# Performance work log

Measured on AMD Instinct MI355X. Metric: run time of the kernel, lower is better.

Reference implementation:

```python
import jax, jax.numpy as jnp
import numpy as np

N_NODES = 50000
HEADS = 3
NEG_SLOPE = 0.2


def gat_conv(h, src, dst, W, al, ar, activation):
    # h: [N, in_dim]; W: [in_dim, H*F]; al, ar: [H, F]
    H, F = al.shape
    feat = (h @ W).reshape(N_NODES, H, F)              # [N, H, F]
    el = jnp.einsum('nhf,hf->nh', feat, al)            # [N, H]
    er = jnp.einsum('nhf,hf->nh', feat, ar)            # [N, H]
    e = jax.nn.leaky_relu(el[src] + er[dst], NEG_SLOPE)  # [E, H]
    # segment softmax over incoming edges of each dst node
    emax = jax.ops.segment_max(e, dst, num_segments=N_NODES)  # [N, H]
    ex = jnp.exp(e - emax[dst])                        # [E, H]
    denom = jax.ops.segment_sum(ex, dst, num_segments=N_NODES)  # [N, H]
    alpha = ex / denom[dst]                            # [E, H]
    msg = feat[src] * alpha[:, :, None]                # [E, H, F]
    out = jax.ops.segment_sum(msg, dst, num_segments=N_NODES)   # [N, H, F]
    if activation is not None:
        out = activation(out)
    return out


def setup_inputs() -> dict:
    key = jax.random.key(0)
    ks = jax.random.split(key, 12)
    n_edges = 1_600_000
    in_dim, hid, heads, n_cls = 256, 64, 3, 40
    d1 = hid * heads  # 192

    def glorot(k, shape):
        fan = shape[0] + shape[-1]
        return jax.random.normal(k, shape, dtype=jnp.float32) * jnp.sqrt(2.0 / fan)

    return {
        'x': jax.random.normal(ks[0], (N_NODES, in_dim), dtype=jnp.float32),
        'src': jax.random.randint(ks[1], (n_edges,), 0, N_NODES),
        'dst': jax.random.randint(ks[2], (n_edges,), 0, N_NODES),
        'W0': glorot(ks[3], (in_dim, heads * hid)),
        'al0': glorot(ks[4], (heads, hid)),
        'ar0': glorot(ks[5], (heads, hid)),
        'W1': glorot(ks[6], (d1, heads * hid)),
        'al1': glorot(ks[7], (heads, hid)),
        'ar1': glorot(ks[8], (heads, hid)),
        'W2': glorot(ks[9], (d1, heads * n_cls)),
        'al2': glorot(ks[10], (heads, n_cls)),
        'ar2': glorot(ks[11], (heads, n_cls)),
    }


def reference(x, src, dst, W0, al0, ar0, W1, al1, ar1, W2, al2, ar2):
    h = gat_conv(x, src, dst, W0, al0, ar0, jax.nn.relu)
    h = h.reshape(N_NODES, -1)  # flatten heads: [N, H*F]
    h = gat_conv(h, src, dst, W1, al1, ar1, jax.nn.relu)
    h = h.reshape(N_NODES, -1)
    logits = gat_conv(h, src, dst, W2, al2, ar2, None).mean(axis=1)  # [N, n_cls]
    return logits
```

## Files before the change

kernel.cpp:

```cpp
#include <hip/hip_runtime.h>

#define NNODES 50000
#define HEADS 3
#define NBUCK 196
#define BCAP  16320

typedef __attribute__((ext_vector_type(8))) short bf16x8;
typedef __attribute__((ext_vector_type(4))) float f32x4;

__device__ __forceinline__ float wred_sum(float v){
  #pragma unroll
  for (int s = 32; s > 0; s >>= 1) v += __shfl_xor(v, s, 64);
  return v;
}
__device__ __forceinline__ unsigned short f2bf(float x){
  unsigned int u = __float_as_uint(x);
  unsigned int r = (u + 0x7FFFu + ((u >> 16) & 1u)) >> 16;
  return (unsigned short)r;
}

__global__ __launch_bounds__(256) void prep_b_all_kernel(
    const float* __restrict__ W0, const float* __restrict__ al0, const float* __restrict__ ar0,
    const float* __restrict__ W1, const float* __restrict__ al1, const float* __restrict__ ar1,
    const float* __restrict__ W2, const float* __restrict__ al2, const float* __restrict__ ar2,
    unsigned short* __restrict__ BfAll)
{
  const int layer = blockIdx.y;
  const float *W, *al, *ar;
  int K, NT, NCf, F; unsigned short* Bf;
  if (layer == 0) { W=W0; al=al0; ar=ar0; K=256; NT=13; NCf=192; F=64; Bf=BfAll; }
  else if (layer == 1) { W=W1; al=al1; ar=ar1; K=192; NT=13; NCf=192; F=64; Bf=BfAll+53248; }
  else { W=W2; al=al2; ar=ar2; K=192; NT=8; NCf=120; F=40; Bf=BfAll+93184; }

  int tid = blockIdx.x * 256 + threadIdx.x;
  int total = (K >> 5) * NT * 64;
  if (tid >= total) return;
  int l  = tid & 63;
  int t  = (tid >> 6) % NT;
  int kc = tid / (NT * 64);
  int k0  = kc * 32 + (l >> 4) * 8;
  int col = t * 16 + (l & 15);
  unsigned short o[8];
  #pragma unroll
  for (int j = 0; j < 8; ++j) {
    int k = k0 + j;
    float v = 0.f;
    if (col < NCf) {
      v = W[(size_t)k * NCf + col];
    } else if (col < NCf + 6) {
      int c = col - NCf;
      int h = (c < 3) ? c : c - 3;
      const float* av = ((c < 3) ? al : ar) + h * F;
      const float* wp = W + (size_t)k * NCf + h * F;
      float a = 0.f;
      for (int f = 0; f < F; ++f) a += wp[f] * av[f];
      v = a;
    }
    o[j] = f2bf(v);
  }
  ushort4* dst = (ushort4*)&Bf[(size_t)tid * 8];
  dst[0] = make_ushort4(o[0], o[1], o[2], o[3]);
  dst[1] = make_ushort4(o[4], o[5], o[6], o[7]);
}

template<int AF32>
__global__ __launch_bounds__(256) void gemm_mfma_kernel(
    const void* __restrict__ Ap, const unsigned short* __restrict__ Bf,
    unsigned short* __restrict__ Cb, float* __restrict__ elp, float* __restrict__ erp,
    int M, int K, int NT, int NCf)
{
  const int w = threadIdx.x >> 6, l = threadIdx.x & 63;
  const int lrow = l & 15, kg = l >> 4;
  const int r0 = blockIdx.x * 64;
  const bf16x8* Bfv = (const bf16x8*)Bf;

  f32x4 acc[4][4];
  #pragma unroll
  for (int mt = 0; mt < 4; ++mt)
    #pragma unroll
    for (int j = 0; j < 4; ++j)
      acc[mt][j] = (f32x4){0.f, 0.f, 0.f, 0.f};

  const int nkc = K >> 5;

#define LOAD_AF(DST, KC) { \
    _Pragma("unroll") \
    for (int mt = 0; mt < 4; ++mt) { \
      int row = r0 + mt * 16 + lrow; \
      bf16x8 z = {0,0,0,0,0,0,0,0}; \
      DST[mt] = z; \
      if (row < M) { \
        if (AF32) { \
          const float* Af = (const float*)Ap; \
          const float4 v0 = *(const float4*)&Af[(size_t)row * K + (KC) * 32 + kg * 8]; \
          const float4 v1 = *(const float4*)&Af[(size_t)row * K + (KC) * 32 + kg * 8 + 4]; \
          bf16x8 a; \
          a[0] = (short)f2bf(v0.x); a[1] = (short)f2bf(v0.y); \
          a[2] = (short)f2bf(v0.z); a[3] = (short)f2bf(v0.w); \
          a[4] = (short)f2bf(v1.x); a[5] = (short)f2bf(v1.y); \
          a[6] = (short)f2bf(v1.z); a[7] = (short)f2bf(v1.w); \
          DST[mt] = a; \
        } else { \
          const unsigned short* Ab = (const unsigned short*)Ap; \
          DST[mt] = *(const bf16x8*)&Ab[(size_t)row * K + (KC) * 32 + kg * 8]; \
        } \
      } \
    } }

  bf16x8 af[4], afn[4];
  LOAD_AF(af, 0)
  for (int kc = 0; kc < nkc; ++kc) {
    if (kc + 1 < nkc) LOAD_AF(afn, kc + 1)
    #pragma unroll
    for (int j = 0; j < 4; ++j) {
      int tile = w + 4 * j;
      if (tile < NT) {
        bf16x8 bfr = Bfv[((size_t)kc * NT + tile) * 64 + l];
        #pragma unroll
        for (int mt = 0; mt < 4; ++mt)
          acc[mt][j] = __builtin_amdgcn_mfma_f32_16x16x32_bf16(af[mt], bfr, acc[mt][j], 0, 0, 0);
      }
    }
    #pragma unroll
    for (int mt = 0; mt < 4; ++mt) af[mt] = afn[mt];
  }
#undef LOAD_AF

  #pragma unroll
  for (int j = 0; j < 4; ++j) {
    int tile = w + 4 * j;
    if (tile >= NT) continue;
    int c = tile * 16 + lrow;
    #pragma unroll
    for (int mt = 0; mt < 4; ++mt) {
      #pragma unroll
      for (int rr = 0; rr < 4; ++rr) {
        int row = r0 + mt * 16 + kg * 4 + rr;
        float v = acc[mt][j][rr];
        float v1 = __shfl_xor(v, 1, 64);
        unsigned p01 = (unsigned)f2bf(v) | ((unsigned)f2bf(v1) << 16);
        unsigned p23 = __shfl_xor(p01, 2, 64);
        if (row < M) {
          if ((lrow & 3) == 0 && c + 3 < NCf)
            *(uint2*)&Cb[(size_t)row * NCf + c] = make_uint2(p01, p23);
          else if (c >= NCf && c < NCf + 3)       elp[row * 4 + (c - NCf)] = v;
          else if (c >= NCf + 3 && c < NCf + 6)   erp[row * 4 + (c - NCf - 3)] = v;
        }
      }
    }
  }
}

__global__ __launch_bounds__(256) void partition_kernel(
    const int* __restrict__ src, const int* __restrict__ dst,
    int* __restrict__ bcur, uint2* __restrict__ ebuf, int E)
{
  __shared__ int hist[NBUCK];
  __shared__ int gbase[NBUCK];
  const int t = threadIdx.x;
  const int e0 = blockIdx.x * 2048;
  for (int i = t; i < NBUCK; i += 256) hist[i] = 0;
  __syncthreads();
  int  b_[8], r_[8];
  uint2 p_[8];
  #pragma unroll
  for (int v = 0; v < 8; ++v) {
    int e = e0 + v * 256 + t;
    b_[v] = -1;
    if (e < E) {
      int s = src[e], d = dst[e];
      p_[v] = make_uint2((unsigned)s, (unsigned)d);
      b_[v] = d >> 8;
      r_[v] = atomicAdd(&hist[b_[v]], 1);
    }
  }
  __syncthreads();
  for (int i = t; i < NBUCK; i += 256) {
    int h = hist[i];
    gbase[i] = h ? atomicAdd(&bcur[i], h) : 0;
  }
  __syncthreads();
  #pragma unroll
  for (int v = 0; v < 8; ++v)
    if (b_[v] >= 0)
      ebuf[(size_t)b_[v] * BCAP + gbase[b_[v]] + r_[v]] = p_[v];
}

__global__ __launch_bounds__(256) void fill_local_kernel(
    const uint2* __restrict__ ebuf, const int* __restrict__ bcur,
    int* __restrict__ off, int* __restrict__ adj, int N)
{
  __shared__ int lhist[256], loff[256], lcur[256];
  __shared__ int wsum[4];
  __shared__ int sbase;
  const int b = blockIdx.x;
  const int t = threadIdx.x;
  const int wv = t >> 6, l = t & 63;
  const int cnt = bcur[b];
  const uint2* seg = ebuf + (size_t)b * BCAP;

  {
    int v = (t < NBUCK) ? bcur[t] : 0;
    int x = v;
    #pragma unroll
    for (int s = 1; s < 64; s <<= 1) {
      int y = __shfl_up(x, s, 64);
      if (l >= s) x += y;
    }
    if (l == 63) wsum[wv] = x;
    lhist[t] = 0; lcur[t] = 0;
    __syncthreads();
    int woff = 0;
    #pragma unroll
    for (int k = 0; k < 4; ++k) woff += (k < wv) ? wsum[k] : 0;
    if (t == b) sbase = woff + x - v;
  }
  __syncthreads();

  for (int i = t; i < cnt; i += 256)
    atomicAdd(&lhist[seg[i].y & 255], 1);
  __syncthreads();

  int v = lhist[t];
  int x = v;
  #pragma unroll
  for (int s = 1; s < 64; s <<= 1) {
    int y = __shfl_up(x, s, 64);
    if (l >= s) x += y;
  }
  if (l == 63) wsum[wv] = x;
  __syncthreads();
  int woff = 0;
  #pragma unroll
  for (int k = 0; k < 4; ++k) woff += (k < wv) ? wsum[k] : 0;
  loff[t] = woff + x - v;
  int gd = (b << 8) + t;
  if (gd <= N) off[gd] = sbase + loff[t];
  __syncthreads();
  const int base = sbase;
  for (int i = t; i < cnt; i += 256) {
    uint2 p = seg[i];
    int d = p.y & 255;
    int r = atomicAdd(&lcur[d], 1);
    adj[base + loff[d] + r] = (int)p.x;
  }
}

__global__ __launch_bounds__(256) void aggregate_kernel(
    const unsigned short* __restrict__ featb, const int* __restrict__ adj,
    const int* __restrict__ off, const float* __restrict__ elp,
    const float* __restrict__ erp, void* __restrict__ outp,
    int N, int F, int mode)
{
  __shared__ float4 pl[4][64];
  int wv = threadIdx.x >> 6, l = threadIdx.x & 63;
  int n  = blockIdx.x * 4 + wv;
  if (n >= N) return;
  const int NC = HEADS * F;
  const unsigned rowbytes = NC * 2;
  int o0 = off[n], d = off[n + 1] - o0;
  float er0 = erp[n * 4 + 0], er1 = erp[n * 4 + 1], er2 = erp[n * 4 + 2];
  const float4* elv = (const float4*)elp;
  const char* fbase = (const char*)featb;
  const int gl = (F == 64) ? 48 : 30;
  const int h  = (F == 64) ? (l >> 4) : (l / 10);
  const unsigned loff2 = (unsigned)l * 8u;
  const float4* plw = pl[wv];

  float s0 = 0.f, s1 = 0.f, s2 = 0.f;
  float4 acc = {0.f, 0.f, 0.f, 0.f};

#define LDU(AA) (*(const uint2*)(fbase + (__float_as_uint((AA).x) + loff2)))
#define FMA4(AA, UU) { \
    float ww = (h == 0) ? (AA).y : (h == 1) ? (AA).z : (AA).w; \
    acc.x += ww * __uint_as_float((UU).x << 16); \
    acc.y += ww * __uint_as_float((UU).x & 0xffff0000u); \
    acc.z += ww * __uint_as_float((UU).y << 16); \
    acc.w += ww * __uint_as_float((UU).y & 0xffff0000u); }

  for (int base = 0; base < d; base += 64) {
    int i = base + l;
    float p0 = 0.f, p1 = 0.f, p2 = 0.f;
    unsigned boff = 0;
    if (i < d) {
      int ssrc = adj[o0 + i];
      boff = (unsigned)ssrc * rowbytes;
      float4 ev = elv[ssrc];
      float x0 = ev.x + er0; x0 = fmaxf(x0, 0.2f * x0);
      float x1 = ev.y + er1; x1 = fmaxf(x1, 0.2f * x1);
      float x2 = ev.z + er2; x2 = fmaxf(x2, 0.2f * x2);
      p0 = __expf(x0); p1 = __expf(x1); p2 = __expf(x2);
    }
    s0 += p0; s1 += p1; s2 += p2;
    pl[wv][l] = make_float4(__uint_as_float(boff), p0, p1, p2);

    int cnt = min(64, d - base);
    if (l < gl) {
      int e = 0;
      if (cnt >= 8) {
        float4 a0 = plw[0], a1 = plw[1], a2 = plw[2], a3 = plw[3];
        uint2 u0 = LDU(a0), u1 = LDU(a1), u2 = LDU(a2), u3 = LDU(a3);
        for (e = 4; e + 4 <= cnt; e += 4) {
          float4 b0 = plw[e], b1 = plw[e + 1], b2 = plw[e + 2], b3 = plw[e + 3];
          uint2 n0 = LDU(b0), n1 = LDU(b1), n2 = LDU(b2), n3 = LDU(b3);
          FMA4(a0, u0) FMA4(a1, u1) FMA4(a2, u2) FMA4(a3, u3)
          a0 = b0; a1 = b1; a2 = b2; a3 = b3;
          u0 = n0; u1 = n1; u2 = n2; u3 = n3;
        }
        FMA4(a0, u0) FMA4(a1, u1) FMA4(a2, u2) FMA4(a3, u3)
      }
      for (; e < cnt; ++e) {
        float4 a0 = plw[e];
        uint2 u0 = LDU(a0);
        FMA4(a0, u0)
      }
    }
  }
#undef LDU
#undef FMA4

  s0 = wred_sum(s0); s1 = wred_sum(s1); s2 = wred_sum(s2);
  float i0 = s0 > 0.f ? 1.f / s0 : 0.f;
  float i1 = s1 > 0.f ? 1.f / s1 : 0.f;
  float i2 = s2 > 0.f ? 1.f / s2 : 0.f;
  float ih = (h == 0) ? i0 : (h == 1) ? i1 : i2;
  acc.x *= ih; acc.y *= ih; acc.z *= ih; acc.w *= ih;

  if (mode == 0) {
    if (l < 48) {
      ushort4 o;
      o.x = f2bf(fmaxf(acc.x, 0.f)); o.y = f2bf(fmaxf(acc.y, 0.f));
      o.z = f2bf(fmaxf(acc.z, 0.f)); o.w = f2bf(fmaxf(acc.w, 0.f));
      *(ushort4*)((unsigned short*)outp + (size_t)n * 192 + l * 4) = o;
    }
  } else {
    float bx = __shfl(acc.x, l + 10, 64), cx = __shfl(acc.x, l + 20, 64);
    float by = __shfl(acc.y, l + 10, 64), cy = __shfl(acc.y, l + 20, 64);
    float bz = __shfl(acc.z, l + 10, 64), cz = __shfl(acc.z, l + 20, 64);
    float bw = __shfl(acc.w, l + 10, 64), cw = __shfl(acc.w, l + 20, 64);
    if (l < 10) {
      float4 o;
      o.x = (acc.x + bx + cx) * (1.f / 3.f);
      o.y = (acc.y + by + cy) * (1.f / 3.f);
      o.z = (acc.z + bz + cz) * (1.f / 3.f);
      o.w = (acc.w + bw + cw) * (1.f / 3.f);
      *(float4*)((float*)outp + (size_t)n * 40 + l * 4) = o;
    }
  }
}

extern "C" void kernel_launch(void* const* d_in, const int* in_sizes, int n_in,
                              void* d_out, int out_size, void* d_ws, size_t ws_size,
                              hipStream_t stream) {
  const float* x   = (const float*)d_in[0];
  const int*   src = (const int*)d_in[1];
  const int*   dst = (const int*)d_in[2];
  const float* W0  = (const float*)d_in[3];
  const float* al0 = (const float*)d_in[4];
  const float* ar0 = (const float*)d_in[5];
  const float* W1  = (const float*)d_in[6];
  const float* al1 = (const float*)d_in[7];
  const float* ar1 = (const float*)d_in[8];
  const float* W2  = (const float*)d_in[9];
  const float* al2 = (const float*)d_in[10];
  const float* ar2 = (const float*)d_in[11];
  const int N = NNODES;
  const int E = in_sizes[1];
  float* out = (float*)d_out;

  char* w = (char*)d_ws;
  uint2*          ebuf  = (uint2*)w;          w += (size_t)NBUCK * BCAP * 8;
  unsigned short* featb = (unsigned short*)w; w += (size_t)N * 192 * 2;
  unsigned short* aggb  = (unsigned short*)w; w += (size_t)N * 192 * 2;
  unsigned short* Bf    = (unsigned short*)w; w += (size_t)256 * 1024;
  float* elp = (float*)w; w += (size_t)N * 4 * 4;
  float* erp = (float*)w; w += (size_t)N * 4 * 4;
  int* off   = (int*)w;  w += (size_t)(N + 1) * 4;
  int* adj   = (int*)w;  w += (size_t)E * 4;
  int* bcur  = (int*)w;  w += (size_t)NBUCK * 4;

  hipMemsetAsync(bcur, 0, (size_t)NBUCK * 4, stream);
  partition_kernel<<<(E + 2047) / 2048, 256, 0, stream>>>(src, dst, bcur, ebuf, E);
  fill_local_kernel<<<NBUCK, 256, 0, stream>>>(ebuf, bcur, off, adj, N);

  prep_b_all_kernel<<<dim3(26, 3), 256, 0, stream>>>(W0, al0, ar0, W1, al1, ar1,
                                                     W2, al2, ar2, Bf);

  int gblk = (N + 63) / 64;
  int ablk = (N + 3) / 4;

  gemm_mfma_kernel<1><<<gblk, 256, 0, stream>>>(x, Bf, featb, elp, erp, N, 256, 13, 192);
  aggregate_kernel<<<ablk, 256, 0, stream>>>(featb, adj, off, elp, erp, aggb, N, 64, 0);
  gemm_mfma_kernel<0><<<gblk, 256, 0, stream>>>(aggb, Bf + 53248, featb, elp, erp, N, 192, 13, 192);
  aggregate_kernel<<<ablk, 256, 0, stream>>>(featb, adj, off, elp, erp, aggb, N, 64, 0);
  gemm_mfma_kernel<0><<<gblk, 256, 0, stream>>>(aggb, Bf + 93184, featb, elp, erp, N, 192, 8, 120);
  aggregate_kernel<<<ablk, 256, 0, stream>>>(featb, adj, off, elp, erp, out, N, 40, 1);
}
```

Measured before the change: 473.2 us.

## Stage A tiles in swizzled LDS and pre-convert input to bf16

Adds a separate kernel that converts x to bf16 up front. The GEMM is templated on K and now loads the whole 64-row A tile into XOR-swizzled shared memory with coalesced 16-byte loads, then reads fragments from LDS while double-buffering the B fragments from global memory. The workspace is reorganised so the edge partition buffer aliases the bf16 x buffer, and padding is added so the unguarded tail-block reads stay in bounds. The goal is to replace strided per-lane global A loads, and the in-GEMM fp32-to-bf16 conversion, with coalesced staging. The cost is an extra conversion pass over x, plus the bf16 write and re-read that pass adds.

```diff
diff --git a/kernel.cpp b/kernel.cpp
--- a/kernel.cpp
+++ b/kernel.cpp
@@ -17,6 +17,17 @@
   unsigned int u = __float_as_uint(x);
   unsigned int r = (u + 0x7FFFu + ((u >> 16) & 1u)) >> 16;
   return (unsigned short)r;
+}
+
+__global__ __launch_bounds__(256) void cvt_bf16_kernel(
+    const float* __restrict__ in, unsigned short* __restrict__ outb, int n4)
+{
+  int i = blockIdx.x * 256 + threadIdx.x;
+  if (i >= n4) return;
+  float4 v = ((const float4*)in)[i];
+  ushort4 o;
+  o.x = f2bf(v.x); o.y = f2bf(v.y); o.z = f2bf(v.z); o.w = f2bf(v.w);
+  ((ushort4*)outb)[i] = o;
 }
 
 __global__ __launch_bounds__(256) void prep_b_all_kernel(
@@ -63,17 +74,33 @@
   dst[1] = make_ushort4(o[4], o[5], o[6], o[7]);
 }
 
-template<int AF32>
+template<int KK>
 __global__ __launch_bounds__(256) void gemm_mfma_kernel(
-    const void* __restrict__ Ap, const unsigned short* __restrict__ Bf,
+    const unsigned short* __restrict__ Ab, const unsigned short* __restrict__ Bf,
     unsigned short* __restrict__ Cb, float* __restrict__ elp, float* __restrict__ erp,
-    int M, int K, int NT, int NCf)
-{
-  const int w = threadIdx.x >> 6, l = threadIdx.x & 63;
+    int M, int NT, int NCf)
+{
+  constexpr int ROWB = KK * 2;
+  __shared__ unsigned short atile[64 * KK];
+  const int t = threadIdx.x;
+  const int w = t >> 6, l = t & 63;
   const int lrow = l & 15, kg = l >> 4;
   const int r0 = blockIdx.x * 64;
   const bf16x8* Bfv = (const bf16x8*)Bf;
 
+  {
+    const char* gsrc = (const char*)(Ab + (size_t)r0 * KK);
+    char* lbase = (char*)atile;
+    #pragma unroll
+    for (int i = 0; i < (64 * ROWB) / 4096; ++i) {
+      int o = i * 4096 + t * 16;
+      int row = o / ROWB;
+      int colb = o - row * ROWB;
+      uint4 v = *(const uint4*)(gsrc + o);
+      *(uint4*)(lbase + row * ROWB + (colb ^ ((row & 7) << 4))) = v;
+    }
+  }
+
   f32x4 acc[4][4];
   #pragma unroll
   for (int mt = 0; mt < 4; ++mt)
@@ -81,50 +108,45 @@
     for (int j = 0; j < 4; ++j)
       acc[mt][j] = (f32x4){0.f, 0.f, 0.f, 0.f};
 
-  const int nkc = K >> 5;
-
-#define LOAD_AF(DST, KC) { \
-    _Pragma("unroll") \
-    for (int mt = 0; mt < 4; ++mt) { \
-      int row = r0 + mt * 16 + lrow; \
-      bf16x8 z = {0,0,0,0,0,0,0,0}; \
-      DST[mt] = z; \
-      if (row < M) { \
-        if (AF32) { \
-          const float* Af = (const float*)Ap; \
-          const float4 v0 = *(const float4*)&Af[(size_t)row * K + (KC) * 32 + kg * 8]; \
-          const float4 v1 = *(const float4*)&Af[(size_t)row * K + (KC) * 32 + kg * 8 + 4]; \
-          bf16x8 a; \
-          a[0] = (short)f2bf(v0.x); a[1] = (short)f2bf(v0.y); \
-          a[2] = (short)f2bf(v0.z); a[3] = (short)f2bf(v0.w); \
-          a[4] = (short)f2bf(v1.x); a[5] = (short)f2bf(v1.y); \
-          a[6] = (short)f2bf(v1.z); a[7] = (short)f2bf(v1.w); \
-          DST[mt] = a; \
-        } else { \
-          const unsigned short* Ab = (const unsigned short*)Ap; \
-          DST[mt] = *(const bf16x8*)&Ab[(size_t)row * K + (KC) * 32 + kg * 8]; \
-        } \
-      } \
-    } }
-
-  bf16x8 af[4], afn[4];
-  LOAD_AF(af, 0)
+  constexpr int nkc = KK / 32;
+  const bf16x8 bz = {0,0,0,0,0,0,0,0};
+
+  __syncthreads();
+
+  bf16x8 bcur[4], bnext[4];
+  #pragma unroll
+  for (int j = 0; j < 4; ++j) {
+    int tile = w + 4 * j;
+    bcur[j] = (tile < NT) ? Bfv[(size_t)tile * 64 + l] : bz;
+  }
+
   for (int kc = 0; kc < nkc; ++kc) {
-    if (kc + 1 < nkc) LOAD_AF(afn, kc + 1)
+    if (kc + 1 < nkc) {
+      #pragma unroll
+      for (int j = 0; j < 4; ++j) {
+        int tile = w + 4 * j;
+        bnext[j] = (tile < NT) ? Bfv[((size_t)(kc + 1) * NT + tile) * 64 + l] : bz;
+      }
+    }
+    bf16x8 af[4];
+    #pragma unroll
+    for (int mt = 0; mt < 4; ++mt) {
+      int row_l = mt * 16 + lrow;
+      int colb  = kc * 64 + kg * 16;
+      af[mt] = *(const bf16x8*)((const char*)atile + row_l * ROWB + (colb ^ ((row_l & 7) << 4)));
+    }
     #pragma unroll
     for (int j = 0; j < 4; ++j) {
       int tile = w + 4 * j;
       if (tile < NT) {
-        bf16x8 bfr = Bfv[((size_t)kc * NT + tile) * 64 + l];
         #pragma unroll
         for (int mt = 0; mt < 4; ++mt)
-          acc[mt][j] = __builtin_amdgcn_mfma_f32_16x16x32_bf16(af[mt], bfr, acc[mt][j], 0, 0, 0);
+          acc[mt][j] = __builtin_amdgcn_mfma_f32_16x16x32_bf16(af[mt], bcur[j], acc[mt][j], 0, 0, 0);
       }
     }
     #pragma unroll
-    for (int mt = 0; mt < 4; ++mt) af[mt] = afn[mt];
-  }
-#undef LOAD_AF
+    for (int j = 0; j < 4; ++j) bcur[j] = bnext[j];
+  }
 
   #pragma unroll
   for (int j = 0; j < 4; ++j) {
@@ -369,30 +391,33 @@
   float* out = (float*)d_out;
 
   char* w = (char*)d_ws;
-  uint2*          ebuf  = (uint2*)w;          w += (size_t)NBUCK * BCAP * 8;
+  unsigned short* xb    = (unsigned short*)w; w += (size_t)N * 256 * 2 + 65536;
   unsigned short* featb = (unsigned short*)w; w += (size_t)N * 192 * 2;
-  unsigned short* aggb  = (unsigned short*)w; w += (size_t)N * 192 * 2;
+  unsigned short* aggb  = (unsigned short*)w; w += (size_t)N * 192 * 2 + 65536;
   unsigned short* Bf    = (unsigned short*)w; w += (size_t)256 * 1024;
   float* elp = (float*)w; w += (size_t)N * 4 * 4;
   float* erp = (float*)w; w += (size_t)N * 4 * 4;
   int* off   = (int*)w;  w += (size_t)(N + 1) * 4;
   int* adj   = (int*)w;  w += (size_t)E * 4;
   int* bcur  = (int*)w;  w += (size_t)NBUCK * 4;
+  uint2* ebuf = (uint2*)xb;
 
   hipMemsetAsync(bcur, 0, (size_t)NBUCK * 4, stream);
   partition_kernel<<<(E + 2047) / 2048, 256, 0, stream>>>(src, dst, bcur, ebuf, E);
   fill_local_kernel<<<NBUCK, 256, 0, stream>>>(ebuf, bcur, off, adj, N);
 
+  cvt_bf16_kernel<<<(N * 256 / 4 + 255) / 256, 256, 0, stream>>>(x, xb, N * 256 / 4);
+
   prep_b_all_kernel<<<dim3(26, 3), 256, 0, stream>>>(W0, al0, ar0, W1, al1, ar1,
                                                      W2, al2, ar2, Bf);
 
   int gblk = (N + 63) / 64;
   int ablk = (N + 3) / 4;
 
-  gemm_mfma_kernel<1><<<gblk, 256, 0, stream>>>(x, Bf, featb, elp, erp, N, 256, 13, 192);
+  gemm_mfma_kernel<256><<<gblk, 256, 0, stream>>>(xb, Bf, featb, elp, erp, N, 13, 192);
   aggregate_kernel<<<ablk, 256, 0, stream>>>(featb, adj, off, elp, erp, aggb, N, 64, 0);
-  gemm_mfma_kernel<0><<<gblk, 256, 0, stream>>>(aggb, Bf + 53248, featb, elp, erp, N, 192, 13, 192);
+  gemm_mfma_kernel<192><<<gblk, 256, 0, stream>>>(aggb, Bf + 53248, featb, elp, erp, N, 13, 192);
   aggregate_kernel<<<ablk, 256, 0, stream>>>(featb, adj, off, elp, erp, aggb, N, 64, 0);
-  gemm_mfma_kernel<0><<<gblk, 256, 0, stream>>>(aggb, Bf + 93184, featb, elp, erp, N, 192, 8, 120);
+  gemm_mfma_kernel<192><<<gblk, 256, 0, stream>>>(aggb, Bf + 93184, featb, elp, erp, N, 8, 120);
   aggregate_kernel<<<ablk, 256, 0, stream>>>(featb, adj, off, elp, erp, out, N, 40, 1);
 }
```

Measured after the change: 431.9 us. 1.1x faster.
